# Optimization experiments

Measured on AMD Instinct MI355X. Metric: run time of the kernel, lower is better.

The kernel has to match this reference:

```python
import jax, jax.numpy as jnp
import numpy as np

TRUST_W, SIM_W, STALE_W = 0.4, 0.4, 0.2
EPS = 1e-8  # torch cosine_similarity norm clamp


def setup_inputs() -> dict:
    key = jax.random.key(0)
    ks = jax.random.split(key, 6)
    B, D, E, C = 8192, 1024, 32, 256
    x = jax.random.normal(ks[0], (B, D), dtype=jnp.float32)
    expert_features = jax.random.normal(ks[1], (E, D), dtype=jnp.float32)
    trust = jax.random.uniform(ks[2], (E,), dtype=jnp.float32)
    staleness = jax.random.uniform(ks[3], (E,), dtype=jnp.float32)
    W = jax.random.normal(ks[4], (E, C, D), dtype=jnp.float32) * 0.02
    b = jax.random.normal(ks[5], (E, C), dtype=jnp.float32) * 0.02
    return {"x": x, "expert_features": expert_features, "trust": trust,
            "staleness": staleness, "W": W, "b": b, "k": 4}


def reference(x, expert_features, trust, staleness, W, b, k):
    # --- scoring: trust + cosine similarity + staleness, per (token, expert) ---
    xn = x / jnp.maximum(jnp.linalg.norm(x, axis=-1, keepdims=True), EPS)
    efn = expert_features / jnp.maximum(
        jnp.linalg.norm(expert_features, axis=-1, keepdims=True), EPS)
    cos = xn @ efn.T                              # [B, E]
    sim = (cos + 1.0) * 0.5
    stale_score = jnp.maximum(0.0, 1.0 - staleness)  # [E]
    scores = TRUST_W * trust + SIM_W * sim + STALE_W * stale_score  # [B, E]

    # --- top-k expert selection per token ---
    _, idx = jax.lax.top_k(scores, k)             # [B, k] int32

    # --- grouped expert heads: dense all-expert GEMM, then gather top-k ---
    all_out = jnp.einsum('bd,ecd->bec', x, W) + b  # [B, E, C]
    sel = jnp.take_along_axis(all_out, idx[:, :, None], axis=1)  # [B, k, C]
    return sel.mean(axis=1)                        # [B, C]
```

## Files before the change

kernel.cpp:

```cpp
#include <hip/hip_runtime.h>
#include <math.h>

#define KMAX 8
#define CSTRIDE 64

typedef short s16x8 __attribute__((ext_vector_type(8)));
typedef float f32x4 __attribute__((ext_vector_type(4)));

__device__ inline ushort f2bf(float f) {
    union { float f; unsigned u; } v; v.f = f;
    unsigned r = v.u + 0x7fffu + ((v.u >> 16) & 1u);
    return (ushort)(r >> 16);
}
__device__ inline float bf2f(ushort b) {
    union { unsigned u; float f; } v; v.u = ((unsigned)b) << 16; return v.f;
}

__device__ inline void gload_lds16(const void* g, void* l) {
    __builtin_amdgcn_global_load_lds(
        (const __attribute__((address_space(1))) unsigned int*)g,
        (__attribute__((address_space(3))) unsigned int*)l, 16, 0, 0);
}

__global__ void k_efnorm(const float* __restrict__ ef, int D,
                         double* __restrict__ efn, int* __restrict__ counts) {
    int e = blockIdx.x;
    int lane = threadIdx.x;
    if (lane == 0) counts[e * CSTRIDE] = 0;
    double s = 0.0;
    for (int i = lane; i < D; i += 64) {
        double v = (double)ef[(size_t)e * D + i];
        s = fma(v, v, s);
    }
    #pragma unroll
    for (int off = 32; off > 0; off >>= 1) s += __shfl_xor(s, off);
    if (lane == 0) efn[e] = sqrt(s);
}

__global__ __launch_bounds__(256) void k_prep_w(
    const float* __restrict__ W, const int* __restrict__ counts,
    int perExpF4, ushort* __restrict__ wbf, int* __restrict__ offs) {
    int e = blockIdx.y;
    if (blockIdx.x == 0 && e == 0 && threadIdx.x == 0) {
        int s = 0;
        for (int e2 = 0; e2 < 32; ++e2) { offs[e2] = s; s += counts[e2 * CSTRIDE]; }
    }
    if (counts[e * CSTRIDE] == 0) return;
    size_t base = (size_t)e * perExpF4;
    #pragma unroll
    for (int j = 0; j < 4; ++j) {
        int idx = (blockIdx.x * 4 + j) * 256 + threadIdx.x;
        if (idx < perExpF4) {
            float4 v = *(const float4*)&W[(base + idx) * 4];
            ushort4 u;
            u.x = f2bf(v.x); u.y = f2bf(v.y); u.z = f2bf(v.z); u.w = f2bf(v.w);
            *(ushort4*)&wbf[(base + idx) * 4] = u;
        }
    }
}

__global__ __launch_bounds__(256) void k_scores3a(
    const float* __restrict__ x, const float* __restrict__ ef,
    int D, int B, int nSB4, ushort* __restrict__ xbf,
    double* __restrict__ pacc, double* __restrict__ paxx,
    double* __restrict__ efn, int* __restrict__ counts)
{
    __shared__ float xs[16 * 64];
    __shared__ float efs[32 * 64];
    __shared__ double wsum[4];

    int tid = threadIdx.x;

    if ((int)blockIdx.x >= nSB4) {
        int e = blockIdx.x - nSB4;
        if (tid == 0) counts[e * CSTRIDE] = 0;
        double s = 0.0;
        for (int i = tid; i < D; i += 256) {
            double v = (double)ef[(size_t)e * D + i];
            s = fma(v, v, s);
        }
        #pragma unroll
        for (int off = 32; off > 0; off >>= 1) s += __shfl_xor(s, off);
        if ((tid & 63) == 0) wsum[tid >> 6] = s;
        __syncthreads();
        if (tid == 0) efn[e] = sqrt(wsum[0] + wsum[1] + wsum[2] + wsum[3]);
        return;
    }

    int tp = tid >> 4, eg = tid & 15;
    int g = blockIdx.x >> 2, h = blockIdx.x & 3;
    int tb = g * 16;
    int kbase = h * (D >> 2);
    int nch = D >> 8;

    int rx = tid >> 4, qx = tid & 15;
    int re0 = tid >> 4, re1 = 16 + (tid >> 4);
    int qe = tid & 15;

    float4 vx  = *(const float4*)&x[(size_t)(tb + rx) * D + kbase + qx * 4];
    float4 ve0 = *(const float4*)&ef[(size_t)re0 * D + kbase + qe * 4];
    float4 ve1 = *(const float4*)&ef[(size_t)re1 * D + kbase + qe * 4];

    double acc0 = 0.0, acc1 = 0.0, axx = 0.0;

    for (int ch = 0; ch < nch; ++ch) {
        int k0 = kbase + ch * 64;
        *(float4*)&xs[rx * 64 + ((qx ^ rx) << 2)] = vx;
        {
            ushort4 u;
            u.x = f2bf(vx.x); u.y = f2bf(vx.y); u.z = f2bf(vx.z); u.w = f2bf(vx.w);
            *(ushort4*)&xbf[(size_t)(tb + rx) * D + k0 + qx * 4] = u;
        }
        *(float4*)&efs[re0 * 64 + ((qe ^ (re0 & 15)) << 2)] = ve0;
        *(float4*)&efs[re1 * 64 + ((qe ^ (re1 & 15)) << 2)] = ve1;
        __syncthreads();

        if (ch + 1 < nch) {
            int k1 = kbase + (ch + 1) * 64;
            vx  = *(const float4*)&x[(size_t)(tb + rx) * D + k1 + qx * 4];
            ve0 = *(const float4*)&ef[(size_t)re0 * D + k1 + qe * 4];
            ve1 = *(const float4*)&ef[(size_t)re1 * D + k1 + qe * 4];
        }

        float a0 = 0.f, a1 = 0.f, ax = 0.f;
        #pragma unroll
        for (int q = 0; q < 16; ++q) {
            float4 xv = *(const float4*)&xs[tp * 64 + ((q ^ tp) << 2)];
            float4 e0 = *(const float4*)&efs[eg * 64 + ((q ^ eg) << 2)];
            float4 e1 = *(const float4*)&efs[(eg + 16) * 64 + ((q ^ eg) << 2)];
            a0 = fmaf(xv.x, e0.x, a0); a0 = fmaf(xv.y, e0.y, a0);
            a0 = fmaf(xv.z, e0.z, a0); a0 = fmaf(xv.w, e0.w, a0);
            a1 = fmaf(xv.x, e1.x, a1); a1 = fmaf(xv.y, e1.y, a1);
            a1 = fmaf(xv.z, e1.z, a1); a1 = fmaf(xv.w, e1.w, a1);
            ax = fmaf(xv.x, xv.x, ax); ax = fmaf(xv.y, xv.y, ax);
            ax = fmaf(xv.z, xv.z, ax); ax = fmaf(xv.w, xv.w, ax);
        }
        __syncthreads();
        acc0 += (double)a0; acc1 += (double)a1; axx += (double)ax;
    }

    int tt = tb + tp;
    pacc[(size_t)(h * 32 + eg) * B + tt] = acc0;
    pacc[(size_t)(h * 32 + eg + 16) * B + tt] = acc1;
    if (eg == 0) paxx[(size_t)h * B + tt] = axx;
}

__global__ __launch_bounds__(256) void k_scores3b(
    const float* __restrict__ trust, const float* __restrict__ stale,
    const double* __restrict__ efn, const double* __restrict__ pacc,
    const double* __restrict__ paxx, const int* __restrict__ kp,
    int B, int* __restrict__ counts, int* __restrict__ lists,
    int* __restrict__ sel)
{
    __shared__ double sc[128 * 33];
    __shared__ int bcnt[32];
    __shared__ int bbase[32];
    __shared__ unsigned char selb[128 * KMAX];
    __shared__ unsigned char lposb[128 * KMAX];

    int tid = threadIdx.x;
    int tk = tid & 127, eh = tid >> 7;
    int t = blockIdx.x * 128 + tk;

    if (tid < 32) bcnt[tid] = 0;

    double axx = (paxx[t] + paxx[(size_t)B + t])
               + (paxx[(size_t)2 * B + t] + paxx[(size_t)3 * B + t]);
    double xn = fmax(sqrt(axx), 1e-8);
    #pragma unroll
    for (int j = 0; j < 16; ++j) {
        int e = eh * 16 + j;
        double dot = (pacc[(size_t)e * B + t] + pacc[(size_t)(32 + e) * B + t])
                   + (pacc[(size_t)(64 + e) * B + t] + pacc[(size_t)(96 + e) * B + t]);
        double en = fmax(efn[e], 1e-8);
        sc[tk * 33 + e] = 0.4 * (double)trust[e]
            + 0.2 * (dot / (xn * en) + 1.0)
            + 0.2 * fmax(0.0, 1.0 - (double)stale[e]);
    }
    __syncthreads();

    int kk = kp[0]; kk = kk < 1 ? 1 : (kk > KMAX ? KMAX : kk);

    if (tid < 128) {
        unsigned mask = 0;
        for (int p = 0; p < kk; ++p) {
            double bv = -1e300; int be = 0;
            #pragma unroll
            for (int e = 0; e < 32; ++e) {
                double v = sc[tid * 33 + e];
                if (!((mask >> e) & 1u) && v > bv) { bv = v; be = e; }
            }
            mask |= 1u << be;
            selb[tid * KMAX + p] = (unsigned char)be;
            lposb[tid * KMAX + p] = (unsigned char)atomicAdd(&bcnt[be], 1);
        }
    }
    __syncthreads();
    if (tid < 32) {
        int c = bcnt[tid];
        bbase[tid] = c ? atomicAdd(&counts[tid * CSTRIDE], c) : 0;
    }
    __syncthreads();
    if (tid < 128) {
        int tt = blockIdx.x * 128 + tid;
        for (int p = 0; p < kk; ++p) {
            int e = selb[tid * KMAX + p];
            int pos = bbase[e] + lposb[tid * KMAX + p];
            lists[(size_t)e * B + pos] = tt;
            sel[(size_t)tt * KMAX + p] = (e << 24) | pos;
        }
    }
}

__global__ __launch_bounds__(512) void k_moe3(
    const ushort* __restrict__ xbf, const ushort* __restrict__ wbf,
    const float* __restrict__ bias, const int* __restrict__ lists,
    const int* __restrict__ counts, const int* __restrict__ offs,
    const int* __restrict__ kp, int B, int C, int D,
    int usePart, ushort* __restrict__ part, float* __restrict__ out)
{
    int e = blockIdx.z;
    int cnt = counts[e * CSTRIDE];
    int row0 = blockIdx.x * 128;
    if (row0 >= cnt) return;
    int col0 = blockIdx.y * 128;
    int nt = min(128, cnt - row0);

    __shared__ ushort xs[128 * 64];
    __shared__ ushort wsh[128 * 64];
    __shared__ int toks[128];

    int tid = threadIdx.x;
    if (tid < 128) toks[tid] = (tid < nt) ? lists[(size_t)e * B + row0 + tid] : 0;
    __syncthreads();

    int lane = tid & 63, wid = tid >> 6;
    int wr = wid >> 1, wc = wid & 1;
    int l15 = lane & 15, l16 = lane >> 4;

    f32x4 acc[2][4];
    #pragma unroll
    for (int m = 0; m < 2; ++m)
        #pragma unroll
        for (int n = 0; n < 4; ++n) acc[m][n] = (f32x4){0.f, 0.f, 0.f, 0.f};

    int nch = D / 64;
    for (int ch = 0; ch < nch; ++ch) {
        int k0 = ch * 64;
        #pragma unroll
        for (int t = 0; t < 2; ++t) {
            int id = t * 512 + tid;
            int r = id >> 3, seg = id & 7;
            int ssw = (seg ^ (r & 7)) << 3;
            gload_lds16(&xbf[(size_t)toks[r] * D + k0 + ssw],
                        (char*)xs + (size_t)(t * 512 + wid * 64) * 16);
        }
        #pragma unroll
        for (int t = 0; t < 2; ++t) {
            int id = t * 512 + tid;
            int r = id >> 3, seg = id & 7;
            int ssw = (seg ^ (r & 7)) << 3;
            gload_lds16(&wbf[((size_t)e * C + col0 + r) * D + k0 + ssw],
                        (char*)wsh + (size_t)(t * 512 + wid * 64) * 16);
        }
        __syncthreads();
        #pragma unroll
        for (int ks = 0; ks < 2; ++ks) {
            s16x8 a[2], bfr[4];
            int sbase = ks * 4 + l16;
            #pragma unroll
            for (int m = 0; m < 2; ++m) {
                int r = wr * 32 + m * 16 + l15;
                a[m] = *(const s16x8*)&xs[r * 64 + ((sbase ^ (l15 & 7)) << 3)];
            }
            #pragma unroll
            for (int n = 0; n < 4; ++n) {
                int r = wc * 64 + n * 16 + l15;
                bfr[n] = *(const s16x8*)&wsh[r * 64 + ((sbase ^ (l15 & 7)) << 3)];
            }
            #pragma unroll
            for (int m = 0; m < 2; ++m)
                #pragma unroll
                for (int n = 0; n < 4; ++n)
                    acc[m][n] = __builtin_amdgcn_mfma_f32_16x16x32_bf16(
                        a[m], bfr[n], acc[m][n], 0, 0, 0);
        }
        __syncthreads();
    }

    int kk = kp[0]; kk = kk < 1 ? 1 : (kk > KMAX ? KMAX : kk);
    if (usePart) {
        int slotBase = offs[e] + row0;
        #pragma unroll
        for (int m = 0; m < 2; ++m) {
            int rbase = wr * 32 + m * 16 + l16 * 4;
            #pragma unroll
            for (int n = 0; n < 4; ++n) {
                int col = col0 + wc * 64 + n * 16 + l15;
                float bv = bias[(size_t)e * C + col];
                #pragma unroll
                for (int r = 0; r < 4; ++r) {
                    int rl = rbase + r;
                    if (rl < nt)
                        part[(size_t)(slotBase + rl) * C + col] =
                            f2bf(acc[m][n][r] + bv);
                }
            }
        }
    } else {
        float invk = 1.0f / (float)kk;
        #pragma unroll
        for (int m = 0; m < 2; ++m) {
            int rbase = wr * 32 + m * 16 + l16 * 4;
            #pragma unroll
            for (int n = 0; n < 4; ++n) {
                int col = col0 + wc * 64 + n * 16 + l15;
                float bv = bias[(size_t)e * C + col];
                #pragma unroll
                for (int r = 0; r < 4; ++r) {
                    int rl = rbase + r;
                    if (rl < nt)
                        atomicAdd(&out[(size_t)toks[rl] * C + col],
                                  invk * (acc[m][n][r] + bv));
                }
            }
        }
    }
}

__global__ __launch_bounds__(256) void k_combine(
    const ushort* __restrict__ part, const int* __restrict__ sel,
    const int* __restrict__ offs, const int* __restrict__ kp,
    int C, float* __restrict__ out)
{
    int kk = kp[0]; kk = kk < 1 ? 1 : (kk > KMAX ? KMAX : kk);
    float invk = 1.0f / (float)kk;
    int sub = threadIdx.x >> 6, lane = threadIdx.x & 63;
    int t = blockIdx.x * 4 + sub;
    for (int c = lane * 4; c < C; c += 256) {
        float s0 = 0.f, s1 = 0.f, s2 = 0.f, s3 = 0.f;
        for (int p = 0; p < kk; ++p) {
            int sv = sel[(size_t)t * KMAX + p];
            int slot = offs[sv >> 24] + (sv & 0xFFFFFF);
            ushort4 u = *(const ushort4*)&part[(size_t)slot * C + c];
            s0 += bf2f(u.x); s1 += bf2f(u.y); s2 += bf2f(u.z); s3 += bf2f(u.w);
        }
        float4 o = make_float4(invk * s0, invk * s1, invk * s2, invk * s3);
        *(float4*)&out[(size_t)t * C + c] = o;
    }
}

__global__ __launch_bounds__(256) void k_scores_legacy(
    const float* __restrict__ x, const float* __restrict__ ef,
    const float* __restrict__ trust, const float* __restrict__ stale,
    const double* __restrict__ efn, const int* __restrict__ kp,
    int D, int B, int* __restrict__ counts, int* __restrict__ lists)
{
    __shared__ float xs[32][72];
    __shared__ float efs[32][72];
    __shared__ double sc[32][33];

    int tid = threadIdx.x;
    int tl = tid >> 3, eg = tid & 7;
    int tb = blockIdx.x * 32;

    double acc[4] = {0, 0, 0, 0};
    double axx = 0.0;
    int nch = D / 64;

    for (int ch = 0; ch < nch; ++ch) {
        #pragma unroll
        for (int t = 0; t < 2; ++t) {
            int id = t * 256 + tid;
            int r = id >> 4, q = id & 15;
            float4 v = *(const float4*)&x[(size_t)(tb + r) * D + ch * 64 + q * 4];
            *(float4*)&xs[r][q * 4] = v;
            float4 w = *(const float4*)&ef[(size_t)r * D + ch * 64 + q * 4];
            *(float4*)&efs[r][q * 4] = w;
        }
        __syncthreads();
        #pragma unroll 4
        for (int q = 0; q < 16; ++q) {
            float4 xv = *(const float4*)&xs[tl][q * 4];
            double x0 = xv.x, x1 = xv.y, x2 = xv.z, x3 = xv.w;
            axx = fma(x0, x0, fma(x1, x1, fma(x2, x2, fma(x3, x3, axx))));
            #pragma unroll
            for (int j = 0; j < 4; ++j) {
                float4 ev = *(const float4*)&efs[eg + 8 * j][q * 4];
                acc[j] = fma(x0, (double)ev.x, acc[j]);
                acc[j] = fma(x1, (double)ev.y, acc[j]);
                acc[j] = fma(x2, (double)ev.z, acc[j]);
                acc[j] = fma(x3, (double)ev.w, acc[j]);
            }
        }
        __syncthreads();
    }

    double xn = fmax(sqrt(axx), 1e-8);
    #pragma unroll
    for (int j = 0; j < 4; ++j) {
        int e = eg + 8 * j;
        double en = fmax(efn[e], 1e-8);
        double cosv = acc[j] / (xn * en);
        sc[tl][e] = 0.4 * (double)trust[e] + 0.2 * (cosv + 1.0)
                  + 0.2 * fmax(0.0, 1.0 - (double)stale[e]);
    }
    __syncthreads();

    if (tid < 32) {
        int kk = kp[0]; kk = kk < 1 ? 1 : (kk > KMAX ? KMAX : kk);
        unsigned mask = 0;
        int t = tb + tid;
        for (int p = 0; p < kk; ++p) {
            double bv = -1e300; int be = 0;
            #pragma unroll
            for (int e = 0; e < 32; ++e) {
                double v = sc[tid][e];
                if (!((mask >> e) & 1u) && v > bv) { bv = v; be = e; }
            }
            mask |= 1u << be;
            int pos = atomicAdd(&counts[be * CSTRIDE], 1);
            lists[(size_t)be * B + pos] = t;
        }
    }
}

__global__ __launch_bounds__(512) void k_moe_f32(
    const float* __restrict__ x, const float* __restrict__ W,
    const float* __restrict__ bias, const int* __restrict__ lists,
    const int* __restrict__ counts, const int* __restrict__ kp,
    int B, int C, int D, float* __restrict__ out)
{
    int e = blockIdx.z;
    int cnt = counts[e * CSTRIDE];
    int row0 = blockIdx.x * 128;
    if (row0 >= cnt) return;
    int col0 = blockIdx.y * 256;
    int nt = min(128, cnt - row0);

    __shared__ ushort xs[128 * 72];
    __shared__ ushort wsh[256 * 72];
    __shared__ int toks[128];

    int tid = threadIdx.x;
    if (tid < 128) toks[tid] = (tid < nt) ? lists[(size_t)e * B + row0 + tid] : 0;
    __syncthreads();

    int lane = tid & 63, wid = tid >> 6;
    int wr = wid >> 2, wc = wid & 3;
    int l15 = lane & 15, l16 = lane >> 4;

    f32x4 acc[4][4];
    #pragma unroll
    for (int m = 0; m < 4; ++m)
        #pragma unroll
        for (int n = 0; n < 4; ++n) acc[m][n] = (f32x4){0.f, 0.f, 0.f, 0.f};

    int nch = D / 64;
    for (int ch = 0; ch < nch; ++ch) {
        int k0 = ch * 64;
        #pragma unroll
        for (int t = 0; t < 4; ++t) {
            int id = t * 512 + tid;
            int r = id >> 4, q = id & 15;
            float4 v = (r < nt)
                ? *(const float4*)&x[(size_t)toks[r] * D + k0 + q * 4]
                : make_float4(0.f, 0.f, 0.f, 0.f);
            ushort4 u;
            u.x = f2bf(v.x); u.y = f2bf(v.y); u.z = f2bf(v.z); u.w = f2bf(v.w);
            *(ushort4*)&xs[r * 72 + q * 4] = u;
        }
        #pragma unroll
        for (int t = 0; t < 8; ++t) {
            int id = t * 512 + tid;
            int r = id >> 4, q = id & 15;
            float4 v = *(const float4*)&W[((size_t)e * C + col0 + r) * D + k0 + q * 4];
            ushort4 u;
            u.x = f2bf(v.x); u.y = f2bf(v.y); u.z = f2bf(v.z); u.w = f2bf(v.w);
            *(ushort4*)&wsh[r * 72 + q * 4] = u;
        }
        __syncthreads();
        #pragma unroll
        for (int ks = 0; ks < 2; ++ks) {
            s16x8 a[4], bfr[4];
            #pragma unroll
            for (int m = 0; m < 4; ++m)
                a[m] = *(const s16x8*)&xs[(wr * 64 + m * 16 + l15) * 72 + ks * 32 + l16 * 8];
            #pragma unroll
            for (int n = 0; n < 4; ++n)
                bfr[n] = *(const s16x8*)&wsh[(wc * 64 + n * 16 + l15) * 72 + ks * 32 + l16 * 8];
            #pragma unroll
            for (int m = 0; m < 4; ++m)
                #pragma unroll
                for (int n = 0; n < 4; ++n)
                    acc[m][n] = __builtin_amdgcn_mfma_f32_16x16x32_bf16(
                        a[m], bfr[n], acc[m][n], 0, 0, 0);
        }
        __syncthreads();
    }

    int kk = kp[0]; kk = kk < 1 ? 1 : (kk > KMAX ? KMAX : kk);
    float invk = 1.0f / (float)kk;
    #pragma unroll
    for (int m = 0; m < 4; ++m) {
        int rbase = wr * 64 + m * 16 + l16 * 4;
        #pragma unroll
        for (int n = 0; n < 4; ++n) {
            int col = col0 + wc * 64 + n * 16 + l15;
            float bv = bias[(size_t)e * C + col];
            #pragma unroll
            for (int r = 0; r < 4; ++r) {
                int rl = rbase + r;
                if (rl < nt)
                    atomicAdd(&out[(size_t)toks[rl] * C + col],
                              invk * (acc[m][n][r] + bv));
            }
        }
    }
}

extern "C" void kernel_launch(void* const* d_in, const int* in_sizes, int n_in,
                              void* d_out, int out_size, void* d_ws, size_t ws_size,
                              hipStream_t stream) {
    const float* x     = (const float*)d_in[0];
    const float* ef    = (const float*)d_in[1];
    const float* trust = (const float*)d_in[2];
    const float* stale = (const float*)d_in[3];
    const float* W     = (const float*)d_in[4];
    const float* b     = (const float*)d_in[5];
    const int*   kp    = (const int*)d_in[6];

    int E = in_sizes[2];
    int D = in_sizes[1] / E;
    int B = in_sizes[0] / D;
    int C = in_sizes[5] / E;
    float* out = (float*)d_out;

    char* ws = (char*)d_ws;
    double* efn   = (double*)ws;
    int*    counts= (int*)(ws + 256);
    size_t off_offs = 256 + 32 * CSTRIDE * 4;
    int*    offs  = (int*)(ws + off_offs);
    size_t off_sel = off_offs + 256;
    int*    sel   = (int*)(ws + off_sel);
    size_t off_lists = off_sel + (size_t)B * KMAX * 4;
    int*    lists = (int*)(ws + off_lists);
    size_t off_pacc = off_lists + (size_t)E * B * 4;
    off_pacc = (off_pacc + 255) & ~(size_t)255;
    double* pacc  = (double*)(ws + off_pacc);
    size_t off_paxx = off_pacc + (size_t)128 * B * 8;
    double* paxx  = (double*)(ws + off_paxx);
    size_t off_xbf = off_paxx + (size_t)4 * B * 8;
    off_xbf = (off_xbf + 255) & ~(size_t)255;
    ushort* xbf = (ushort*)(ws + off_xbf);
    size_t off_wbf = off_xbf + (size_t)B * D * 2;
    ushort* wbf = (ushort*)(ws + off_wbf);
    size_t off_part = off_wbf + (size_t)E * C * D * 2;
    off_part = (off_part + 255) & ~(size_t)255;
    ushort* part = (ushort*)(ws + off_part);
    size_t need_mid  = off_part;
    size_t need_full = off_part + (size_t)B * KMAX * C * 2;

    bool fullPath = ws_size >= need_mid;
    int usePart = (fullPath && ws_size >= need_full) ? 1 : 0;

    if (!usePart)
        hipMemsetAsync(d_out, 0, (size_t)out_size * sizeof(float), stream);

    if (fullPath) {
        int nSB4 = (B / 16) * 4;
        k_scores3a<<<nSB4 + E, 256, 0, stream>>>(x, ef, D, B, nSB4, xbf,
                                                 pacc, paxx, efn, counts);
        k_scores3b<<<B / 128, 256, 0, stream>>>(trust, stale, efn, pacc, paxx,
                                                kp, B, counts, lists, sel);
        int perExpF4 = (C * D) / 4;
        dim3 wgrid((perExpF4 + 1023) / 1024, E);
        k_prep_w<<<wgrid, 256, 0, stream>>>(W, counts, perExpF4, wbf, offs);
        dim3 grid((B + 127) / 128, C / 128, E);
        k_moe3<<<grid, 512, 0, stream>>>(xbf, wbf, b, lists, counts, offs, kp,
                                         B, C, D, usePart, part, out);
        if (usePart)
            k_combine<<<B / 4, 256, 0, stream>>>(part, sel, offs, kp, C, out);
    } else {
        k_efnorm<<<E, 64, 0, stream>>>(ef, D, efn, counts);
        k_scores_legacy<<<B / 32, 256, 0, stream>>>(x, ef, trust, stale, efn,
                                                    kp, D, B, counts, lists);
        dim3 grid((B + 127) / 128, C / 256, E);
        k_moe_f32<<<grid, 512, 0, stream>>>(x, W, b, lists, counts, kp,
                                            B, C, D, out);
    }
}
```

Measured before the change: 78.38 us.

## Split MoE GEMM along K into two halves with partial planes

The grouped expert GEMM now splits the reduction dimension D in two, doubling the number of workgroups. Each half writes its own bf16 partial plane, with the bias added only by the first half, and the combine kernel sums both planes. This aims to raise occupancy when the per-expert tile count is low. The cost is twice the partial-output traffic, an extra bf16 rounding step, and a larger workspace requirement. Because the column index assumes C/128 == 2, the change is only correct for C=256; the atomic fallback path also relies on that layout.

```diff
diff --git a/kernel.cpp b/kernel.cpp
--- a/kernel.cpp
+++ b/kernel.cpp
@@ -216,14 +216,16 @@
     const ushort* __restrict__ xbf, const ushort* __restrict__ wbf,
     const float* __restrict__ bias, const int* __restrict__ lists,
     const int* __restrict__ counts, const int* __restrict__ offs,
-    const int* __restrict__ kp, int B, int C, int D,
+    const int* __restrict__ kp, int B, int C, int D, int SLOTS,
     int usePart, ushort* __restrict__ part, float* __restrict__ out)
 {
     int e = blockIdx.z;
     int cnt = counts[e * CSTRIDE];
     int row0 = blockIdx.x * 128;
     if (row0 >= cnt) return;
-    int col0 = blockIdx.y * 128;
+    int col0 = (blockIdx.y & 1) * 128;
+    int kh = blockIdx.y >> 1;
+    int kbase = kh * (D >> 1);
     int nt = min(128, cnt - row0);
 
     __shared__ ushort xs[128 * 64];
@@ -244,9 +246,9 @@
         #pragma unroll
         for (int n = 0; n < 4; ++n) acc[m][n] = (f32x4){0.f, 0.f, 0.f, 0.f};
 
-    int nch = D / 64;
+    int nch = D >> 7;
     for (int ch = 0; ch < nch; ++ch) {
-        int k0 = ch * 64;
+        int k0 = kbase + ch * 64;
         #pragma unroll
         for (int t = 0; t < 2; ++t) {
             int id = t * 512 + tid;
@@ -291,19 +293,20 @@
     int kk = kp[0]; kk = kk < 1 ? 1 : (kk > KMAX ? KMAX : kk);
     if (usePart) {
         int slotBase = offs[e] + row0;
+        size_t plane = (size_t)kh * SLOTS;
         #pragma unroll
         for (int m = 0; m < 2; ++m) {
             int rbase = wr * 32 + m * 16 + l16 * 4;
             #pragma unroll
             for (int n = 0; n < 4; ++n) {
                 int col = col0 + wc * 64 + n * 16 + l15;
-                float bv = bias[(size_t)e * C + col];
+                float badd = (kh == 0) ? bias[(size_t)e * C + col] : 0.f;
                 #pragma unroll
                 for (int r = 0; r < 4; ++r) {
                     int rl = rbase + r;
                     if (rl < nt)
-                        part[(size_t)(slotBase + rl) * C + col] =
-                            f2bf(acc[m][n][r] + bv);
+                        part[(plane + slotBase + rl) * C + col] =
+                            f2bf(acc[m][n][r] + badd);
                 }
             }
         }
@@ -315,13 +318,13 @@
             #pragma unroll
             for (int n = 0; n < 4; ++n) {
                 int col = col0 + wc * 64 + n * 16 + l15;
-                float bv = bias[(size_t)e * C + col];
+                float badd = (kh == 0) ? bias[(size_t)e * C + col] : 0.f;
                 #pragma unroll
                 for (int r = 0; r < 4; ++r) {
                     int rl = rbase + r;
                     if (rl < nt)
                         atomicAdd(&out[(size_t)toks[rl] * C + col],
-                                  invk * (acc[m][n][r] + bv));
+                                  invk * (acc[m][n][r] + badd));
                 }
             }
         }
@@ -331,7 +334,7 @@
 __global__ __launch_bounds__(256) void k_combine(
     const ushort* __restrict__ part, const int* __restrict__ sel,
     const int* __restrict__ offs, const int* __restrict__ kp,
-    int C, float* __restrict__ out)
+    int C, int SLOTS, float* __restrict__ out)
 {
     int kk = kp[0]; kk = kk < 1 ? 1 : (kk > KMAX ? KMAX : kk);
     float invk = 1.0f / (float)kk;
@@ -342,8 +345,12 @@
         for (int p = 0; p < kk; ++p) {
             int sv = sel[(size_t)t * KMAX + p];
             int slot = offs[sv >> 24] + (sv & 0xFFFFFF);
-            ushort4 u = *(const ushort4*)&part[(size_t)slot * C + c];
-            s0 += bf2f(u.x); s1 += bf2f(u.y); s2 += bf2f(u.z); s3 += bf2f(u.w);
+            ushort4 u0 = *(const ushort4*)&part[(size_t)slot * C + c];
+            ushort4 u1 = *(const ushort4*)&part[((size_t)SLOTS + slot) * C + c];
+            s0 += bf2f(u0.x) + bf2f(u1.x);
+            s1 += bf2f(u0.y) + bf2f(u1.y);
+            s2 += bf2f(u0.z) + bf2f(u1.z);
+            s3 += bf2f(u0.w) + bf2f(u1.w);
         }
         float4 o = make_float4(invk * s0, invk * s1, invk * s2, invk * s3);
         *(float4*)&out[(size_t)t * C + c] = o;
@@ -535,6 +542,7 @@
     int B = in_sizes[0] / D;
     int C = in_sizes[5] / E;
     float* out = (float*)d_out;
+    int SLOTS = B * KMAX;
 
     char* ws = (char*)d_ws;
     double* efn   = (double*)ws;
@@ -559,7 +567,7 @@
     off_part = (off_part + 255) & ~(size_t)255;
     ushort* part = (ushort*)(ws + off_part);
     size_t need_mid  = off_part;
-    size_t need_full = off_part + (size_t)B * KMAX * C * 2;
+    size_t need_full = off_part + (size_t)2 * SLOTS * C * 2;
 
     bool fullPath = ws_size >= need_mid;
     int usePart = (fullPath && ws_size >= need_full) ? 1 : 0;
@@ -576,11 +584,12 @@
         int perExpF4 = (C * D) / 4;
         dim3 wgrid((perExpF4 + 1023) / 1024, E);
         k_prep_w<<<wgrid, 256, 0, stream>>>(W, counts, perExpF4, wbf, offs);
-        dim3 grid((B + 127) / 128, C / 128, E);
+        dim3 grid((B + 127) / 128, (C / 128) * 2, E);
         k_moe3<<<grid, 512, 0, stream>>>(xbf, wbf, b, lists, counts, offs, kp,
-                                         B, C, D, usePart, part, out);
+                                         B, C, D, SLOTS, usePart, part, out);
         if (usePart)
-            k_combine<<<B / 4, 256, 0, stream>>>(part, sel, offs, kp, C, out);
+            k_combine<<<B / 4, 256, 0, stream>>>(part, sel, offs, kp, C,
+                                                 SLOTS, out);
     } else {
         k_efnorm<<<E, 64, 0, stream>>>(ef, D, efn, counts);
         k_scores_legacy<<<B / 32, 256, 0, stream>>>(x, ef, trust, stale, efn,
```

Result: slower. 84.89 us (+8.3%).
